# Kernel tuning notes

Hardware: AMD Instinct MI355X
Metric: run time of the kernel (lower is better)

Reference implementation:

```python
import jax, jax.numpy as jnp
import numpy as np

N, D_MODEL, D_FFN, K = 8192, 1024, 4096, 512


def setup_inputs() -> dict:
    key = jax.random.key(0)
    ks = jax.random.split(key, 5)
    x = jax.random.normal(ks[0], (N, D_MODEL), dtype=jnp.float32)
    topk_indices = jax.random.randint(ks[1], (N, K), 0, D_FFN, dtype=jnp.int32)
    scale = 0.02
    w_gate = jax.random.normal(ks[2], (D_MODEL, D_FFN), dtype=jnp.float32) * scale
    w_up = jax.random.normal(ks[3], (D_MODEL, D_FFN), dtype=jnp.float32) * scale
    w_down = jax.random.normal(ks[4], (D_FFN, D_MODEL), dtype=jnp.float32) * scale
    return {"x": x, "topk_indices": topk_indices, "w_gate": w_gate, "w_up": w_up, "w_down": w_down}


def reference(x, topk_indices, w_gate, w_up, w_down):
    # Dense gate/up projections: [N, d_ffn]
    G = x @ w_gate
    U = x @ w_up
    # Gather only the top-k active neurons per token and fuse SwiGLU there.
    G_act = jnp.take_along_axis(G, topk_indices, axis=1)  # [N, k]
    U_act = jnp.take_along_axis(U, topk_indices, axis=1)  # [N, k]
    Z_active = jax.nn.silu(G_act) * U_act                 # [N, k]
    # Sparse-to-dense down projection: scatter active activations back into
    # the d_ffn axis (zeros elsewhere), then dense matmul with w_down.
    n, k = topk_indices.shape
    rows = jnp.arange(n, dtype=topk_indices.dtype)[:, None]
    Z_dense = jnp.zeros((n, w_down.shape[0]), dtype=Z_active.dtype).at[rows, topk_indices].add(Z_active)
    return Z_dense @ w_down  # [N, d_model]
```

## Files before the change

### kernel.cpp

```cpp
#include <hip/hip_runtime.h>
#include <hip/hip_bf16.h>
#include <cstdint>
#include <cstddef>

#define N_TOK   8192
#define D_MODEL 1024
#define D_FFN   4096
#define K_TOP   512
#define NHALF   2048

typedef __bf16 bf16_t;
typedef __bf16 bf16x8 __attribute__((ext_vector_type(8)));
typedef __bf16 bf16x4 __attribute__((ext_vector_type(4)));
typedef float  f32x4  __attribute__((ext_vector_type(4)));


__global__ void cvt_f32_bf16(const float* __restrict__ in, bf16_t* __restrict__ out, int n4) {
  int i = blockIdx.x * blockDim.x + threadIdx.x;
  if (i < n4) {
    const f32x4 v = ((const f32x4*)in)[i];
    bf16x4 o;
    o[0] = (bf16_t)v[0]; o[1] = (bf16_t)v[1]; o[2] = (bf16_t)v[2]; o[3] = (bf16_t)v[3];
    ((bf16x4*)out)[i] = o;
  }
}

__global__ void transpose_cvt(const float* __restrict__ in, bf16_t* __restrict__ out,
                              int rows, int cols) {
  __shared__ float tile[32][33];
  const int tx = threadIdx.x, ty = threadIdx.y;
  const int x = blockIdx.x * 32 + tx;
#pragma unroll
  for (int i = 0; i < 32; i += 8) {
    int y = blockIdx.y * 32 + ty + i;
    tile[ty + i][tx] = in[(size_t)y * cols + x];
  }
  __syncthreads();
  const int xo = blockIdx.y * 32 + tx;
#pragma unroll
  for (int i = 0; i < 32; i += 8) {
    int yo = blockIdx.x * 32 + ty + i;
    out[(size_t)yo * rows + xo] = (bf16_t)tile[tx][ty + i];
  }
}

#define ROWS_PER_BLK 4
__global__ __launch_bounds__(256) void count_scatter_lds(
    const int* __restrict__ idx, unsigned int* __restrict__ M) {
  __shared__ unsigned int loc[ROWS_PER_BLK * (D_FFN / 8)];
  const int t = threadIdx.x;
  const int r0 = blockIdx.x * ROWS_PER_BLK;

#pragma unroll
  for (int i = 0; i < ROWS_PER_BLK * (D_FFN / 8) / 256; ++i)
    loc[t + i * 256] = 0;
  __syncthreads();

  const int* ip = idx + (size_t)r0 * K_TOP;
#pragma unroll
  for (int i = 0; i < ROWS_PER_BLK * K_TOP / 256; ++i) {
    const int e = t + i * 256;
    const int lr = e >> 9;
    const int j = ip[e];
    atomicAdd(&loc[lr * (D_FFN / 8) + (j >> 3)], 1u << ((j & 7) * 4));
  }
  __syncthreads();

  unsigned int* op = M + (size_t)r0 * (D_FFN / 8);
#pragma unroll
  for (int i = 0; i < ROWS_PER_BLK * (D_FFN / 8) / 256; ++i)
    op[t + i * 256] = loc[t + i * 256];
}


__device__ __forceinline__ void gload_lds16(const void* g, void* l) {
#if __has_builtin(__builtin_amdgcn_global_load_lds)
  __builtin_amdgcn_global_load_lds((__attribute__((address_space(1))) void*)(g),
                                   (__attribute__((address_space(3))) void*)(l), 16, 0, 0);
#else
  *(bf16x8*)l = *(const bf16x8*)g;
#endif
}

#define MFMA16(ACC, AF, BF)                                                      \
  _Pragma("unroll")                                                              \
  for (int m = 0; m < 4; ++m)                                                    \
    _Pragma("unroll")                                                            \
    for (int n = 0; n < 4; ++n)                                                  \
      ACC[m][n] = __builtin_amdgcn_mfma_f32_16x16x32_bf16(AF[m], BF[n], ACC[m][n], 0, 0, 0);

#define PHASE_SYNC_PRE()                                                         \
  __builtin_amdgcn_s_barrier();                                                  \
  asm volatile("s_waitcnt lgkmcnt(0)" ::: "memory");                             \
  __builtin_amdgcn_sched_barrier(0);                                             \
  __builtin_amdgcn_s_setprio(1);

#define PHASE_SYNC_POST()                                                        \
  __builtin_amdgcn_s_setprio(0);                                                 \
  __builtin_amdgcn_s_barrier();

#define BM1 256
#define BN1 128
#define BK1 64
#define NT1 (D_MODEL / BK1)
#define LDSBUF 65536

__global__ __launch_bounds__(512, 2) void gemm_gateup_8p(
    const bf16_t* __restrict__ A,
    const bf16_t* __restrict__ Bg,
    const bf16_t* __restrict__ Bu,
    const unsigned int* __restrict__ cnt,
    bf16_t* __restrict__ Z,
    int n_base)
{
  extern __shared__ char smem[];
  const int t = threadIdx.x;
  const int lane = t & 63;
  const int w = t >> 6;
  const int wr = w >> 1;
  const int wc = w & 1;
  const int l15 = lane & 15;
  const int grp = lane >> 4;
  const int m0 = blockIdx.x * BM1;
  const int n0 = blockIdx.y * BN1;

  int offA[4], offB[2];
#pragma unroll
  for (int c = 0; c < 4; ++c) {
    const int s = c * 512 + w * 64 + lane;
    const int r = s >> 3, cb = (s & 7) ^ (r & 7);
    offA[c] = (m0 + r) * D_MODEL + cb * 8;
  }
#pragma unroll
  for (int c = 0; c < 2; ++c) {
    const int s = c * 512 + w * 64 + lane;
    const int r = s >> 3, cb = (s & 7) ^ (r & 7);
    offB[c] = (n_base + n0 + r) * D_MODEL + cb * 8;
  }
  const int dst0 = (w * 64 + lane) * 16;

  const int swz = l15 & 7;
  const int a_k0 = wr * 8192 + l15 * 128 + ((0 + grp) ^ swz) * 16;
  const int a_k1 = wr * 8192 + l15 * 128 + ((4 + grp) ^ swz) * 16;
  const int bg_k0 = 32768 + wc * 8192 + l15 * 128 + ((0 + grp) ^ swz) * 16;
  const int bg_k1 = 32768 + wc * 8192 + l15 * 128 + ((4 + grp) ^ swz) * 16;
  const int bu_k0 = bg_k0 + 16384;
  const int bu_k1 = bg_k1 + 16384;

#pragma unroll
  for (int c = 0; c < 4; ++c) gload_lds16(A + offA[c], smem + dst0 + c * 8192);
#pragma unroll
  for (int c = 0; c < 2; ++c) gload_lds16(Bg + offB[c], smem + 32768 + dst0 + c * 8192);
#pragma unroll
  for (int c = 0; c < 2; ++c) gload_lds16(Bu + offB[c], smem + 49152 + dst0 + c * 8192);
  asm volatile("s_waitcnt vmcnt(0)" ::: "memory");
  __builtin_amdgcn_s_barrier();

  f32x4 accg[4][4] = {};
  f32x4 accu[4][4] = {};

  for (int tt = 0; tt < NT1; ++tt) {
    char* rb = smem + (tt & 1) * LDSBUF;
    char* wb = smem + ((tt & 1) ^ 1) * LDSBUF;
    const int kg = (tt + 1) * BK1;
    const bool st = (tt + 1 < NT1);
    bf16x8 af[4], bgf[4], buf_[4];

#pragma unroll
    for (int m = 0; m < 4; ++m) af[m] = *(const bf16x8*)(rb + a_k0 + m * 2048);
#pragma unroll
    for (int n = 0; n < 4; ++n) bgf[n] = *(const bf16x8*)(rb + bg_k0 + n * 2048);
    if (st) {
#pragma unroll
      for (int c = 0; c < 4; ++c) gload_lds16(A + offA[c] + kg, wb + dst0 + c * 8192);
#pragma unroll
      for (int c = 0; c < 2; ++c) gload_lds16(Bg + offB[c] + kg, wb + 32768 + dst0 + c * 8192);
#pragma unroll
      for (int c = 0; c < 2; ++c) gload_lds16(Bu + offB[c] + kg, wb + 49152 + dst0 + c * 8192);
    }
    PHASE_SYNC_PRE();
    MFMA16(accg, af, bgf);
    PHASE_SYNC_POST();

#pragma unroll
    for (int n = 0; n < 4; ++n) buf_[n] = *(const bf16x8*)(rb + bu_k0 + n * 2048);
    PHASE_SYNC_PRE();
    MFMA16(accu, af, buf_);
    PHASE_SYNC_POST();

#pragma unroll
    for (int m = 0; m < 4; ++m) af[m] = *(const bf16x8*)(rb + a_k1 + m * 2048);
#pragma unroll
    for (int n = 0; n < 4; ++n) bgf[n] = *(const bf16x8*)(rb + bg_k1 + n * 2048);
    PHASE_SYNC_PRE();
    MFMA16(accg, af, bgf);
    PHASE_SYNC_POST();

#pragma unroll
    for (int n = 0; n < 4; ++n) buf_[n] = *(const bf16x8*)(rb + bu_k1 + n * 2048);
    __builtin_amdgcn_s_barrier();
    asm volatile("s_waitcnt lgkmcnt(0)" ::: "memory");
    __builtin_amdgcn_sched_barrier(0);
    __builtin_amdgcn_s_setprio(1);
    MFMA16(accu, af, buf_);
    __builtin_amdgcn_s_setprio(0);
    if (st) asm volatile("s_waitcnt vmcnt(0)" ::: "memory");
    __builtin_amdgcn_s_barrier();
  }

#pragma unroll
  for (int m = 0; m < 4; ++m) {
#pragma unroll
    for (int n = 0; n < 4; ++n) {
      const int colL = n0 + wc * 64 + n * 16 + l15;
      const int jg = n_base + colL;
#pragma unroll
      for (int j = 0; j < 4; ++j) {
        const int row = m0 + wr * 64 + m * 16 + grp * 4 + j;
        float g = accg[m][n][j];
        float u = accu[m][n][j];
        unsigned int cw = cnt[(size_t)row * (D_FFN / 8) + (jg >> 3)];
        float c = (float)((cw >> ((jg & 7) * 4)) & 15u);
        float z = c * u * (g / (1.0f + __expf(-g)));
        Z[(size_t)row * NHALF + colL] = (bf16_t)z;
      }
    }
  }
}

#define BM2 256
#define BN2 128
#define BK2 64
#define NT2 (NHALF / BK2)
#define LDSBUF2 49152

__global__ __launch_bounds__(512, 2) void gemm_down_8p(
    const bf16_t* __restrict__ A,
    const bf16_t* __restrict__ B,
    float* __restrict__ C,
    int k_base, int accum)
{
  extern __shared__ char smem[];
  const int t = threadIdx.x;
  const int lane = t & 63;
  const int w = t >> 6;
  const int wr = w >> 1;
  const int wc = w & 1;
  const int l15 = lane & 15;
  const int grp = lane >> 4;
  const int m0 = blockIdx.x * BM2;
  const int n0 = blockIdx.y * BN2;

  int offA[4], offB[2];
#pragma unroll
  for (int c = 0; c < 4; ++c) {
    const int s = c * 512 + w * 64 + lane;
    const int r = s >> 3, cb = (s & 7) ^ (r & 7);
    offA[c] = (m0 + r) * NHALF + cb * 8;
  }
#pragma unroll
  for (int c = 0; c < 2; ++c) {
    const int s = c * 512 + w * 64 + lane;
    const int r = s >> 3, cb = (s & 7) ^ (r & 7);
    offB[c] = (n0 + r) * D_FFN + k_base + cb * 8;
  }
  const int dst0 = (w * 64 + lane) * 16;

  const int swz = l15 & 7;
  const int a_k0 = wr * 8192 + l15 * 128 + ((0 + grp) ^ swz) * 16;
  const int a_k1 = wr * 8192 + l15 * 128 + ((4 + grp) ^ swz) * 16;
  const int b_k0 = 32768 + wc * 8192 + l15 * 128 + ((0 + grp) ^ swz) * 16;
  const int b_k1 = 32768 + wc * 8192 + l15 * 128 + ((4 + grp) ^ swz) * 16;

#pragma unroll
  for (int c = 0; c < 4; ++c) gload_lds16(A + offA[c], smem + dst0 + c * 8192);
#pragma unroll
  for (int c = 0; c < 2; ++c) gload_lds16(B + offB[c], smem + 32768 + dst0 + c * 8192);
  asm volatile("s_waitcnt vmcnt(0)" ::: "memory");
  __builtin_amdgcn_s_barrier();

  f32x4 acc[4][4] = {};

  for (int tt = 0; tt < NT2; ++tt) {
    char* rb = smem + (tt & 1) * LDSBUF2;
    char* wb = smem + ((tt & 1) ^ 1) * LDSBUF2;
    const int kg = (tt + 1) * BK2;
    const bool st = (tt + 1 < NT2);
    bf16x8 af[4], bf[4];

#pragma unroll
    for (int m = 0; m < 4; ++m) af[m] = *(const bf16x8*)(rb + a_k0 + m * 2048);
#pragma unroll
    for (int n = 0; n < 4; ++n) bf[n] = *(const bf16x8*)(rb + b_k0 + n * 2048);
    if (st) {
#pragma unroll
      for (int c = 0; c < 4; ++c) gload_lds16(A + offA[c] + kg, wb + dst0 + c * 8192);
#pragma unroll
      for (int c = 0; c < 2; ++c) gload_lds16(B + offB[c] + kg, wb + 32768 + dst0 + c * 8192);
    }
    PHASE_SYNC_PRE();
    MFMA16(acc, af, bf);
    PHASE_SYNC_POST();

#pragma unroll
    for (int m = 0; m < 4; ++m) af[m] = *(const bf16x8*)(rb + a_k1 + m * 2048);
#pragma unroll
    for (int n = 0; n < 4; ++n) bf[n] = *(const bf16x8*)(rb + b_k1 + n * 2048);
    __builtin_amdgcn_s_barrier();
    asm volatile("s_waitcnt lgkmcnt(0)" ::: "memory");
    __builtin_amdgcn_sched_barrier(0);
    __builtin_amdgcn_s_setprio(1);
    MFMA16(acc, af, bf);
    __builtin_amdgcn_s_setprio(0);
    if (st) asm volatile("s_waitcnt vmcnt(0)" ::: "memory");
    __builtin_amdgcn_s_barrier();
  }

#pragma unroll
  for (int m = 0; m < 4; ++m) {
#pragma unroll
    for (int n = 0; n < 4; ++n) {
      const int col = n0 + wc * 64 + n * 16 + l15;
#pragma unroll
      for (int j = 0; j < 4; ++j) {
        const int row = m0 + wr * 64 + m * 16 + grp * 4 + j;
        const size_t off = (size_t)row * D_MODEL + col;
        float prev = accum ? C[off] : 0.0f;
        C[off] = prev + acc[m][n][j];
      }
    }
  }
}


extern "C" void kernel_launch(void* const* d_in, const int* in_sizes, int n_in,
                              void* d_out, int out_size, void* d_ws, size_t ws_size,
                              hipStream_t stream) {
  const float* x  = (const float*)d_in[0];
  const int*   idx = (const int*)d_in[1];
  const float* wg = (const float*)d_in[2];
  const float* wu = (const float*)d_in[3];
  const float* wd = (const float*)d_in[4];
  float* out = (float*)d_out;

  char* ws = (char*)d_ws;
  const size_t SZ_XB  = (size_t)N_TOK * D_MODEL * 2;
  const size_t SZ_W   = (size_t)D_MODEL * D_FFN * 2;
  const size_t SZ_CNT = (size_t)N_TOK * D_FFN / 2;
  bf16_t* xb  = (bf16_t*)(ws);
  bf16_t* wgT = (bf16_t*)(ws + SZ_XB);
  bf16_t* wuT = (bf16_t*)(ws + SZ_XB + SZ_W);
  bf16_t* wdT = (bf16_t*)(ws + SZ_XB + 2 * SZ_W);
  unsigned int* cnt = (unsigned int*)(ws + SZ_XB + 3 * SZ_W);
  bf16_t* Z   = (bf16_t*)(ws + SZ_XB + 3 * SZ_W + SZ_CNT);

  (void)hipFuncSetAttribute((const void*)gemm_gateup_8p,
                            hipFuncAttributeMaxDynamicSharedMemorySize, 131072);
  (void)hipFuncSetAttribute((const void*)gemm_down_8p,
                            hipFuncAttributeMaxDynamicSharedMemorySize, 98304);

  count_scatter_lds<<<N_TOK / ROWS_PER_BLK, 256, 0, stream>>>(idx, cnt);
  cvt_f32_bf16<<<(N_TOK * D_MODEL / 4 + 255) / 256, 256, 0, stream>>>(x, xb, N_TOK * D_MODEL / 4);
  transpose_cvt<<<dim3(D_FFN / 32, D_MODEL / 32), dim3(32, 8), 0, stream>>>(wg, wgT, D_MODEL, D_FFN);
  transpose_cvt<<<dim3(D_FFN / 32, D_MODEL / 32), dim3(32, 8), 0, stream>>>(wu, wuT, D_MODEL, D_FFN);
  transpose_cvt<<<dim3(D_MODEL / 32, D_FFN / 32), dim3(32, 8), 0, stream>>>(wd, wdT, D_FFN, D_MODEL);

  gemm_gateup_8p<<<dim3(N_TOK / BM1, NHALF / BN1), 512, 131072, stream>>>(xb, wgT, wuT, cnt, Z, 0);
  gemm_down_8p<<<dim3(N_TOK / BM2, D_MODEL / BN2), 512, 98304, stream>>>(Z, wdT, out, 0, 0);
  gemm_gateup_8p<<<dim3(N_TOK / BM1, NHALF / BN1), 512, 131072, stream>>>(xb, wgT, wuT, cnt, Z, NHALF);
  gemm_down_8p<<<dim3(N_TOK / BM2, D_MODEL / BN2), 512, 98304, stream>>>(Z, wdT, out, NHALF, 1);
}
```

Baseline: 270.2 us.

## Collapse GEMM phase barriers and remap workgroups across XCDs

```diff
diff --git a/kernel.cpp b/kernel.cpp
--- a/kernel.cpp
+++ b/kernel.cpp
@@ -89,23 +89,13 @@
     for (int n = 0; n < 4; ++n)                                                  \
       ACC[m][n] = __builtin_amdgcn_mfma_f32_16x16x32_bf16(AF[m], BF[n], ACC[m][n], 0, 0, 0);
 
-#define PHASE_SYNC_PRE()                                                         \
-  __builtin_amdgcn_s_barrier();                                                  \
-  asm volatile("s_waitcnt lgkmcnt(0)" ::: "memory");                             \
-  __builtin_amdgcn_sched_barrier(0);                                             \
-  __builtin_amdgcn_s_setprio(1);
-
-#define PHASE_SYNC_POST()                                                        \
-  __builtin_amdgcn_s_setprio(0);                                                 \
-  __builtin_amdgcn_s_barrier();
-
 #define BM1 256
 #define BN1 128
 #define BK1 64
 #define NT1 (D_MODEL / BK1)
 #define LDSBUF 65536
 
-__global__ __launch_bounds__(512, 2) void gemm_gateup_8p(
+__global__ __launch_bounds__(512, 2) void gemm_gateup_2p(
     const bf16_t* __restrict__ A,
     const bf16_t* __restrict__ Bg,
     const bf16_t* __restrict__ Bu,
@@ -121,8 +111,12 @@
   const int wc = w & 1;
   const int l15 = lane & 15;
   const int grp = lane >> 4;
-  const int m0 = blockIdx.x * BM1;
-  const int n0 = blockIdx.y * BN1;
+
+  const int nwg = gridDim.x * gridDim.y;
+  int flat = blockIdx.x + gridDim.x * blockIdx.y;
+  flat = (flat & 7) * (nwg >> 3) + (flat >> 3);
+  const int m0 = (flat % gridDim.x) * BM1;
+  const int n0 = (flat / gridDim.x) * BN1;
 
   int offA[4], offB[2];
 #pragma unroll
@@ -164,12 +158,18 @@
     char* wb = smem + ((tt & 1) ^ 1) * LDSBUF;
     const int kg = (tt + 1) * BK1;
     const bool st = (tt + 1 < NT1);
-    bf16x8 af[4], bgf[4], buf_[4];
-
-#pragma unroll
-    for (int m = 0; m < 4; ++m) af[m] = *(const bf16x8*)(rb + a_k0 + m * 2048);
-#pragma unroll
-    for (int n = 0; n < 4; ++n) bgf[n] = *(const bf16x8*)(rb + bg_k0 + n * 2048);
+    bf16x8 af0[4], af1[4], bg0[4], bg1[4], bu0[4], bu1[4];
+
+#pragma unroll
+    for (int m = 0; m < 4; ++m) {
+      af0[m] = *(const bf16x8*)(rb + a_k0 + m * 2048);
+      af1[m] = *(const bf16x8*)(rb + a_k1 + m * 2048);
+    }
+#pragma unroll
+    for (int n = 0; n < 4; ++n) {
+      bg0[n] = *(const bf16x8*)(rb + bg_k0 + n * 2048);
+      bg1[n] = *(const bf16x8*)(rb + bg_k1 + n * 2048);
+    }
     if (st) {
 #pragma unroll
       for (int c = 0; c < 4; ++c) gload_lds16(A + offA[c] + kg, wb + dst0 + c * 8192);
@@ -178,31 +178,23 @@
 #pragma unroll
       for (int c = 0; c < 2; ++c) gload_lds16(Bu + offB[c] + kg, wb + 49152 + dst0 + c * 8192);
     }
-    PHASE_SYNC_PRE();
-    MFMA16(accg, af, bgf);
-    PHASE_SYNC_POST();
-
-#pragma unroll
-    for (int n = 0; n < 4; ++n) buf_[n] = *(const bf16x8*)(rb + bu_k0 + n * 2048);
-    PHASE_SYNC_PRE();
-    MFMA16(accu, af, buf_);
-    PHASE_SYNC_POST();
-
-#pragma unroll
-    for (int m = 0; m < 4; ++m) af[m] = *(const bf16x8*)(rb + a_k1 + m * 2048);
-#pragma unroll
-    for (int n = 0; n < 4; ++n) bgf[n] = *(const bf16x8*)(rb + bg_k1 + n * 2048);
-    PHASE_SYNC_PRE();
-    MFMA16(accg, af, bgf);
-    PHASE_SYNC_POST();
-
-#pragma unroll
-    for (int n = 0; n < 4; ++n) buf_[n] = *(const bf16x8*)(rb + bu_k1 + n * 2048);
     __builtin_amdgcn_s_barrier();
     asm volatile("s_waitcnt lgkmcnt(0)" ::: "memory");
-    __builtin_amdgcn_sched_barrier(0);
     __builtin_amdgcn_s_setprio(1);
-    MFMA16(accu, af, buf_);
+    MFMA16(accg, af0, bg0);
+    MFMA16(accg, af1, bg1);
+    __builtin_amdgcn_s_setprio(0);
+    __builtin_amdgcn_s_barrier();
+
+#pragma unroll
+    for (int n = 0; n < 4; ++n) {
+      bu0[n] = *(const bf16x8*)(rb + bu_k0 + n * 2048);
+      bu1[n] = *(const bf16x8*)(rb + bu_k1 + n * 2048);
+    }
+    asm volatile("s_waitcnt lgkmcnt(0)" ::: "memory");
+    __builtin_amdgcn_s_setprio(1);
+    MFMA16(accu, af0, bu0);
+    MFMA16(accu, af1, bu1);
     __builtin_amdgcn_s_setprio(0);
     if (st) asm volatile("s_waitcnt vmcnt(0)" ::: "memory");
     __builtin_amdgcn_s_barrier();
@@ -234,7 +226,7 @@
 #define NT2 (NHALF / BK2)
 #define LDSBUF2 49152
 
-__global__ __launch_bounds__(512, 2) void gemm_down_8p(
+__global__ __launch_bounds__(512, 2) void gemm_down_1p(
     const bf16_t* __restrict__ A,
     const bf16_t* __restrict__ B,
     float* __restrict__ C,
@@ -248,8 +240,12 @@
   const int wc = w & 1;
   const int l15 = lane & 15;
   const int grp = lane >> 4;
-  const int m0 = blockIdx.x * BM2;
-  const int n0 = blockIdx.y * BN2;
+
+  const int nwg = gridDim.x * gridDim.y;
+  int flat = blockIdx.x + gridDim.x * blockIdx.y;
+  flat = (flat & 7) * (nwg >> 3) + (flat >> 3);
+  const int m0 = (flat % gridDim.x) * BM2;
+  const int n0 = (flat / gridDim.x) * BN2;
 
   int offA[4], offB[2];
 #pragma unroll
@@ -286,31 +282,29 @@
     char* wb = smem + ((tt & 1) ^ 1) * LDSBUF2;
     const int kg = (tt + 1) * BK2;
     const bool st = (tt + 1 < NT2);
-    bf16x8 af[4], bf[4];
-
-#pragma unroll
-    for (int m = 0; m < 4; ++m) af[m] = *(const bf16x8*)(rb + a_k0 + m * 2048);
-#pragma unroll
-    for (int n = 0; n < 4; ++n) bf[n] = *(const bf16x8*)(rb + b_k0 + n * 2048);
+    bf16x8 af0[4], af1[4], bf0[4], bf1[4];
+
+#pragma unroll
+    for (int m = 0; m < 4; ++m) {
+      af0[m] = *(const bf16x8*)(rb + a_k0 + m * 2048);
+      af1[m] = *(const bf16x8*)(rb + a_k1 + m * 2048);
+    }
+#pragma unroll
+    for (int n = 0; n < 4; ++n) {
+      bf0[n] = *(const bf16x8*)(rb + b_k0 + n * 2048);
+      bf1[n] = *(const bf16x8*)(rb + b_k1 + n * 2048);
+    }
     if (st) {
 #pragma unroll
       for (int c = 0; c < 4; ++c) gload_lds16(A + offA[c] + kg, wb + dst0 + c * 8192);
 #pragma unroll
       for (int c = 0; c < 2; ++c) gload_lds16(B + offB[c] + kg, wb + 32768 + dst0 + c * 8192);
     }
-    PHASE_SYNC_PRE();
-    MFMA16(acc, af, bf);
-    PHASE_SYNC_POST();
-
-#pragma unroll
-    for (int m = 0; m < 4; ++m) af[m] = *(const bf16x8*)(rb + a_k1 + m * 2048);
-#pragma unroll
-    for (int n = 0; n < 4; ++n) bf[n] = *(const bf16x8*)(rb + b_k1 + n * 2048);
     __builtin_amdgcn_s_barrier();
     asm volatile("s_waitcnt lgkmcnt(0)" ::: "memory");
-    __builtin_amdgcn_sched_barrier(0);
     __builtin_amdgcn_s_setprio(1);
-    MFMA16(acc, af, bf);
+    MFMA16(acc, af0, bf0);
+    MFMA16(acc, af1, bf1);
     __builtin_amdgcn_s_setprio(0);
     if (st) asm volatile("s_waitcnt vmcnt(0)" ::: "memory");
     __builtin_amdgcn_s_barrier();
@@ -354,9 +348,9 @@
   unsigned int* cnt = (unsigned int*)(ws + SZ_XB + 3 * SZ_W);
   bf16_t* Z   = (bf16_t*)(ws + SZ_XB + 3 * SZ_W + SZ_CNT);
 
-  (void)hipFuncSetAttribute((const void*)gemm_gateup_8p,
+  (void)hipFuncSetAttribute((const void*)gemm_gateup_2p,
                             hipFuncAttributeMaxDynamicSharedMemorySize, 131072);
-  (void)hipFuncSetAttribute((const void*)gemm_down_8p,
+  (void)hipFuncSetAttribute((const void*)gemm_down_1p,
                             hipFuncAttributeMaxDynamicSharedMemorySize, 98304);
 
   count_scatter_lds<<<N_TOK / ROWS_PER_BLK, 256, 0, stream>>>(idx, cnt);
@@ -365,8 +359,8 @@
   transpose_cvt<<<dim3(D_FFN / 32, D_MODEL / 32), dim3(32, 8), 0, stream>>>(wu, wuT, D_MODEL, D_FFN);
   transpose_cvt<<<dim3(D_MODEL / 32, D_FFN / 32), dim3(32, 8), 0, stream>>>(wd, wdT, D_FFN, D_MODEL);
 
-  gemm_gateup_8p<<<dim3(N_TOK / BM1, NHALF / BN1), 512, 131072, stream>>>(xb, wgT, wuT, cnt, Z, 0);
-  gemm_down_8p<<<dim3(N_TOK / BM2, D_MODEL / BN2), 512, 98304, stream>>>(Z, wdT, out, 0, 0);
-  gemm_gateup_8p<<<dim3(N_TOK / BM1, NHALF / BN1), 512, 131072, stream>>>(xb, wgT, wuT, cnt, Z, NHALF);
-  gemm_down_8p<<<dim3(N_TOK / BM2, D_MODEL / BN2), 512, 98304, stream>>>(Z, wdT, out, NHALF, 1);
-}
+  gemm_gateup_2p<<<dim3(N_TOK / BM1, NHALF / BN1), 512, 131072, stream>>>(xb, wgT, wuT, cnt, Z, 0);
+  gemm_down_1p<<<dim3(N_TOK / BM2, D_MODEL / BN2), 512, 98304, stream>>>(Z, wdT, out, 0, 0);
+  gemm_gateup_2p<<<dim3(N_TOK / BM1, NHALF / BN1), 512, 131072, stream>>>(xb, wgT, wuT, cnt, Z, NHALF);
+  gemm_down_1p<<<dim3(N_TOK / BM2, D_MODEL / BN2), 512, 98304, stream>>>(Z, wdT, out, NHALF, 1);
+}
```

Result: slower. 289.6 us (+7.2%).
